# Kernel tuning notes

Hardware: AMD Instinct MI355X
Metric: run time of the kernel (lower is better)

Reference implementation:

```python
import jax, jax.numpy as jnp
import numpy as np

OUTPUT_DIM = 1024  # init kwarg output_dim


def _adaptive_avg_pool_last(x, out_dim):
    """Faithful F.adaptive_avg_pool1d over the last axis (static shapes)."""
    in_dim = x.shape[-1]
    if in_dim % out_dim == 0:
        k = in_dim // out_dim
        return x.reshape(x.shape[:-1] + (out_dim, k)).mean(axis=-1)
    # generic case: window i covers [floor(i*In/Out), ceil((i+1)*In/Out))
    idx = np.arange(out_dim)
    starts = (idx * in_dim) // out_dim
    ends = -((-(idx + 1) * in_dim) // out_dim)
    W = np.zeros((in_dim, out_dim), dtype=np.float32)
    for i in range(out_dim):
        W[starts[i]:ends[i], i] = 1.0 / (ends[i] - starts[i])
    return x @ jnp.asarray(W)


def _per_layer_gram(feat, output_dim):
    N, C, ph, pw = feat.shape
    P = ph * pw
    c_red = min(C, 64)
    f = feat.reshape(N, C, P).transpose(0, 2, 1)        # [N, P, C]
    f = _adaptive_avg_pool_last(f, c_red)               # [N, P, Cr] channel reduction
    fr = f.transpose(0, 2, 1)                           # [N, Cr, P]
    gram = jnp.einsum('ncp,ndp->ncd', fr, fr) / P       # [N, Cr, Cr] per-patch Gram
    return _adaptive_avg_pool_last(gram.reshape(N, c_red * c_red), output_dim)  # [N, output_dim]


def setup_inputs() -> dict:
    key = jax.random.key(0)
    k0, k1 = jax.random.split(key)
    feat0 = jax.random.normal(k0, (6272, 512, 3, 3), dtype=jnp.float32)
    feat1 = jax.random.normal(k1, (6272, 1024, 3, 3), dtype=jnp.float32)
    return {"feat0": feat0, "feat1": feat1}


def reference(feat0, feat1):
    # stack over layers -> [N, L=2, output_dim]
    return jnp.stack(
        [_per_layer_gram(feat0, OUTPUT_DIM), _per_layer_gram(feat1, OUTPUT_DIM)],
        axis=1,
    )
```

## Files before the change

### kernel.cpp

```cpp
#include <hip/hip_runtime.h>


#define N_SAMPLES 6272

__global__ __launch_bounds__(256, 4) void patchgram_kernel(
    const float* __restrict__ f0, const float* __restrict__ f1,
    float* __restrict__ out)
{
    __shared__ float4 s4[2304];
    __shared__ float  fr[576];
    float* s = (float*)s4;

    const int bid   = blockIdx.x;
    const int n     = bid >> 1;
    const int layer = bid & 1;
    const int t     = threadIdx.x;

    const float* __restrict__ src = layer ? f1 : f0;
    const int C    = layer ? 1024 : 512;
    const int k    = C >> 6;
    const int nflt = C * 9;
    const int nv4  = nflt >> 2;

    const float4* __restrict__ g = (const float4*)(src + (size_t)n * nflt);
    for (int i = t; i < nv4; i += 256) s4[i] = g[i];
    __syncthreads();

    const float rk = 1.0f / (float)k;
    for (int pair = t; pair < 576; pair += 256) {
        const int i = pair / 9;
        const int p = pair - i * 9;
        const float* base = s + i * k * 9 + p;
        float acc = 0.f;
        if (k == 8) {
#pragma unroll
            for (int cc = 0; cc < 8; ++cc) acc += base[cc * 9];
        } else {
#pragma unroll
            for (int cc = 0; cc < 16; ++cc) acc += base[cc * 9];
        }
        fr[pair] = acc * rk;
    }
    __syncthreads();

    const int c0 = (t >> 4) << 2;
    const int dg = t & 15;

    float a[4][9];
#pragma unroll
    for (int i = 0; i < 4; ++i)
#pragma unroll
        for (int p = 0; p < 9; ++p) a[i][p] = fr[(c0 + i) * 9 + p];

    float acc[4] = {0.f, 0.f, 0.f, 0.f};
#pragma unroll
    for (int dd = 0; dd < 4; ++dd) {
        float b[9];
        const int d = dg * 4 + dd;
#pragma unroll
        for (int p = 0; p < 9; ++p) b[p] = fr[d * 9 + p];
#pragma unroll
        for (int i = 0; i < 4; ++i) {
            float s2 = 0.f;
#pragma unroll
            for (int p = 0; p < 9; ++p) s2 += a[i][p] * b[p];
            acc[i] += s2;
        }
    }

    float* __restrict__ o = out + ((size_t)n * 2 + layer) * 1024;
    const float scale = 1.0f / 36.0f;
#pragma unroll
    for (int i = 0; i < 4; ++i) o[(c0 + i) * 16 + dg] = acc[i] * scale;
}

extern "C" void kernel_launch(void* const* d_in, const int* in_sizes, int n_in,
                              void* d_out, int out_size, void* d_ws, size_t ws_size,
                              hipStream_t stream) {
    const float* f0 = (const float*)d_in[0];
    const float* f1 = (const float*)d_in[1];
    float* out = (float*)d_out;
    patchgram_kernel<<<N_SAMPLES * 2, 256, 0, stream>>>(f0, f1, out);
}
```

Measured before the change: 399.0 us.

## Reduce channels in registers and pre-pool Gram columns before the dot product

Each thread now loads 36 contiguous floats directly from global memory and sums them into 9 per-patch values in registers. Partial sums are combined with warp shuffles, so the full per-sample input is no longer staged in shared memory. The output pooling over groups of 4 columns is folded into the Gram product by pre-summing B rows, which cuts the dot products to 4 per thread, and stores become float4. The smaller shared footprint allows a higher occupancy hint, at the cost of an extra sync and less coalesced strided loads.

```diff
diff --git a/kernel.cpp b/kernel.cpp
--- a/kernel.cpp
+++ b/kernel.cpp
@@ -3,13 +3,14 @@
 
 #define N_SAMPLES 6272
 
-__global__ __launch_bounds__(256, 4) void patchgram_kernel(
+__global__ __launch_bounds__(256, 8) void patchgram_kernel(
     const float* __restrict__ f0, const float* __restrict__ f1,
     float* __restrict__ out)
 {
-    __shared__ float4 s4[2304];
-    __shared__ float  fr[576];
-    float* s = (float*)s4;
+    __shared__ float4 fr4[64 * 3];
+    __shared__ float4 B4[16 * 3];
+    float* fr = (float*)fr4;
+    float* B  = (float*)B4;
 
     const int bid   = blockIdx.x;
     const int n     = bid >> 1;
@@ -17,61 +18,73 @@
     const int t     = threadIdx.x;
 
     const float* __restrict__ src = layer ? f1 : f0;
-    const int C    = layer ? 1024 : 512;
-    const int k    = C >> 6;
-    const int nflt = C * 9;
-    const int nv4  = nflt >> 2;
+    const int nflt   = layer ? 9216 : 4608;
+    const int nload  = nflt / 36;
+    const int gshift = layer ? 2 : 1;
 
-    const float4* __restrict__ g = (const float4*)(src + (size_t)n * nflt);
-    for (int i = t; i < nv4; i += 256) s4[i] = g[i];
-    __syncthreads();
+    if (t < nload) {
+        const float4* __restrict__ g =
+            (const float4*)(src + (size_t)n * nflt) + t * 9;
+        float4 v[9];
+#pragma unroll
+        for (int j = 0; j < 9; ++j) v[j] = g[j];
 
-    const float rk = 1.0f / (float)k;
-    for (int pair = t; pair < 576; pair += 256) {
-        const int i = pair / 9;
-        const int p = pair - i * 9;
-        const float* base = s + i * k * 9 + p;
-        float acc = 0.f;
-        if (k == 8) {
+        float acc[9];
 #pragma unroll
-            for (int cc = 0; cc < 8; ++cc) acc += base[cc * 9];
-        } else {
+        for (int p = 0; p < 9; ++p) acc[p] = 0.f;
 #pragma unroll
-            for (int cc = 0; cc < 16; ++cc) acc += base[cc * 9];
+        for (int j = 0; j < 9; ++j) {
+            acc[(4 * j + 0) % 9] += v[j].x;
+            acc[(4 * j + 1) % 9] += v[j].y;
+            acc[(4 * j + 2) % 9] += v[j].z;
+            acc[(4 * j + 3) % 9] += v[j].w;
         }
-        fr[pair] = acc * rk;
+#pragma unroll
+        for (int p = 0; p < 9; ++p) acc[p] += __shfl_xor(acc[p], 1);
+        if (layer) {
+#pragma unroll
+            for (int p = 0; p < 9; ++p) acc[p] += __shfl_xor(acc[p], 2);
+        }
+        if ((t & ((1 << gshift) - 1)) == 0) {
+            const int row = t >> gshift;
+            fr4[row * 3 + 0] = make_float4(acc[0], acc[1], acc[2], acc[3]);
+            fr4[row * 3 + 1] = make_float4(acc[4], acc[5], acc[6], acc[7]);
+            fr4[row * 3 + 2] = make_float4(acc[8], 0.f, 0.f, 0.f);
+        }
     }
     __syncthreads();
 
-    const int c0 = (t >> 4) << 2;
-    const int dg = t & 15;
+    if (t < 144) {
+        const int dg = t / 9;
+        const int p  = t - dg * 9;
+        B[dg * 12 + p] = fr[(4 * dg + 0) * 12 + p] + fr[(4 * dg + 1) * 12 + p] +
+                         fr[(4 * dg + 2) * 12 + p] + fr[(4 * dg + 3) * 12 + p];
+    }
+    __syncthreads();
 
-    float a[4][9];
+    const int c   = t >> 2;
+    const int dgq = t & 3;
+    const float4 a0 = fr4[c * 3 + 0];
+    const float4 a1 = fr4[c * 3 + 1];
+    const float4 a2 = fr4[c * 3 + 2];
+    const int   k     = layer ? 16 : 8;
+    const float scale = 1.0f / (36.0f * (float)(k * k));
+
+    float4 o4;
+    float* op = (float*)&o4;
 #pragma unroll
-    for (int i = 0; i < 4; ++i)
-#pragma unroll
-        for (int p = 0; p < 9; ++p) a[i][p] = fr[(c0 + i) * 9 + p];
-
-    float acc[4] = {0.f, 0.f, 0.f, 0.f};
-#pragma unroll
-    for (int dd = 0; dd < 4; ++dd) {
-        float b[9];
-        const int d = dg * 4 + dd;
-#pragma unroll
-        for (int p = 0; p < 9; ++p) b[p] = fr[d * 9 + p];
-#pragma unroll
-        for (int i = 0; i < 4; ++i) {
-            float s2 = 0.f;
-#pragma unroll
-            for (int p = 0; p < 9; ++p) s2 += a[i][p] * b[p];
-            acc[i] += s2;
-        }
+    for (int j = 0; j < 4; ++j) {
+        const int d = dgq * 4 + j;
+        const float4 b0 = B4[d * 3 + 0];
+        const float4 b1 = B4[d * 3 + 1];
+        const float4 b2 = B4[d * 3 + 2];
+        float s = a0.x * b0.x + a0.y * b0.y + a0.z * b0.z + a0.w * b0.w
+                + a1.x * b1.x + a1.y * b1.y + a1.z * b1.z + a1.w * b1.w
+                + a2.x * b2.x;
+        op[j] = s * scale;
     }
-
-    float* __restrict__ o = out + ((size_t)n * 2 + layer) * 1024;
-    const float scale = 1.0f / 36.0f;
-#pragma unroll
-    for (int i = 0; i < 4; ++i) o[(c0 + i) * 16 + dg] = acc[i] * scale;
+    float4* o = (float4*)(out + ((size_t)n * 2 + layer) * 1024 + c * 16 + dgq * 4);
+    *o = o4;
 }
 
 extern "C" void kernel_launch(void* const* d_in, const int* in_sizes, int n_in,
```

Result: faster. 389.6 us (-2.3%).
